# Optimization experiments

Hardware: AMD Instinct MI355X
Metric: run time of the kernel (lower is better)

Reference implementation:

```python
import jax, jax.numpy as jnp
import numpy as np

NUM_HEADS = 8
DIM_HEAD = 64
EMBED = NUM_HEADS * DIM_HEAD  # 512
B, S, L = 2, 128, 128


def setup_inputs() -> dict:
    key = jax.random.key(0)
    k1, k2 = jax.random.split(key)
    x = jax.random.normal(k1, (B, EMBED, S, L), dtype=jnp.float32)
    # 1x1 Conv2d == pointwise linear over channels: weight [3E, E], bias [3E]
    W = jax.random.normal(k2, (3 * EMBED, EMBED), dtype=jnp.float32) * (EMBED ** -0.5)
    b = jnp.zeros((3 * EMBED,), dtype=jnp.float32)
    return {"x": x, "W": W, "b": b}


def reference(x, W, b):
    Bsz, D, S_, L_ = x.shape
    H, Dh = NUM_HEADS, DIM_HEAD
    scale = Dh ** -0.5
    # QKV projection (1x1 conv)
    qkv = jnp.einsum('oi,bisl->bosl', W, x) + b[None, :, None, None]
    q, k, v = jnp.split(qkv, 3, axis=1)
    q = q.reshape(Bsz, H, Dh, S_, L_) * scale
    k = k.reshape(Bsz, H, Dh, S_, L_)
    v = v.reshape(Bsz, H, Dh, S_, L_)
    # Column attention: attend along S axis, independently per column l
    col_scores = jnp.einsum('bhdsl,bhdtl->bhlst', q, k)      # [B,H,L,S,S]
    col_attn = jax.nn.softmax(col_scores, axis=-1)
    out_col = jnp.einsum('bhlst,bhdtl->bhdsl', col_attn, v)  # [B,H,Dh,S,L]
    # Row attention: attend along L axis, independently per row s
    row_scores = jnp.einsum('bhdsl,bhdsm->bhslm', q, k)      # [B,H,S,L,L]
    row_attn = jax.nn.softmax(row_scores, axis=-1)
    out_row = jnp.einsum('bhslm,bhdsm->bhdsl', row_attn, v)  # [B,H,Dh,S,L]
    out = (out_col + out_row).reshape(Bsz, H * Dh, S_, L_)
    return out
```

## Files before the change

### kernel.cpp

```cpp
#include <hip/hip_runtime.h>
#include <stdint.h>

#define EMB 512
#define THREE_E 1536
#define SL 16384
#define K_DIM 512

typedef unsigned short ushort;
typedef short bf16x8 __attribute__((ext_vector_type(8)));
typedef float f32x4 __attribute__((ext_vector_type(4)));

__device__ __forceinline__ ushort f2bf(float f) {
  unsigned u = __float_as_uint(f);
  u += 0x7fffu + ((u >> 16) & 1u);
  return (ushort)(u >> 16);
}
__device__ __forceinline__ float bf2f(ushort s) {
  return __uint_as_float((unsigned)s << 16);
}

__device__ __forceinline__ void async16(const ushort* g, ushort* l) {
  __builtin_amdgcn_global_load_lds(
      (const __attribute__((address_space(1))) unsigned int*)g,
      (__attribute__((address_space(3))) unsigned int*)l, 16, 0, 0);
}

__global__ __launch_bounds__(256) void prep(const float* __restrict__ W,
                                            ushort* __restrict__ Wb,
                                            const float* __restrict__ x,
                                            ushort* __restrict__ xT) {
  __shared__ ushort t[64][68];
  const int bx = blockIdx.x;
  const int tid = threadIdx.x;
  if (bx < 768) {
    int i = bx * 256 + tid;
    float4 f = ((const float4*)W)[i];
    uint2 o;
    o.x = (unsigned)f2bf(f.x) | ((unsigned)f2bf(f.y) << 16);
    o.y = (unsigned)f2bf(f.z) | ((unsigned)f2bf(f.w) << 16);
    ((uint2*)Wb)[i] = o;
    return;
  }
  const int r = bx - 768;
  const int n0 = (r & 255) * 64;
  const int i0 = ((r >> 8) & 7) * 64;
  const int b = r >> 11;
  const float* xp = x + ((size_t)(b * EMB + i0)) * SL + n0;
  #pragma unroll
  for (int it = 0; it < 4; it++) {
    int f = it * 256 + tid;
    int rr = f >> 4, c4 = (f & 15) * 4;
    float4 v = *(const float4*)&xp[(size_t)rr * SL + c4];
    uint2 p;
    p.x = (unsigned)f2bf(v.x) | ((unsigned)f2bf(v.y) << 16);
    p.y = (unsigned)f2bf(v.z) | ((unsigned)f2bf(v.w) << 16);
    *(uint2*)&t[rr][c4] = p;
  }
  __syncthreads();
  ushort* op = xT + ((size_t)(b * SL + n0)) * EMB + i0;
  #pragma unroll
  for (int it = 0; it < 4; it++) {
    int u = it * 256 + tid;
    int n = u >> 4, i4 = (u & 15) * 4;
    uint2 p;
    ushort* ps = (ushort*)&p;
    #pragma unroll
    for (int j = 0; j < 4; j++) ps[j] = t[i4 + j][n];
    *(uint2*)&op[(size_t)n * EMB + i4] = p;
  }
}

__global__ __launch_bounds__(512, 2) void qkv_gemm(const ushort* __restrict__ Wb,
                                                   const ushort* __restrict__ xT,
                                                   const float* __restrict__ bias,
                                                   ushort* __restrict__ rowQ) {
  __shared__ __align__(16) char sm[131072];
  ushort* const A0 = (ushort*)sm;
  ushort* const B0 = (ushort*)(sm + 32768);
  ushort* const A1 = (ushort*)(sm + 65536);
  ushort* const B1 = (ushort*)(sm + 98304);
  const int tid = threadIdx.x;
  const int bz = blockIdx.z;
  const int m0 = blockIdx.y * 256;
  const int n0 = blockIdx.x * 256;
  const int lane = tid & 63, w = tid >> 6;
  const int wm = w >> 2, wn = w & 3;
  const int l15 = lane & 15, quad = lane >> 4;
  const int r8 = lane >> 3;
  const int cg8 = ((lane & 7) ^ r8) * 8;
  const int rx = l15 & 7;
  const ushort* Wt = Wb + (size_t)m0 * K_DIM;
  const ushort* Xt = xT + ((size_t)bz * SL + n0) * K_DIM;

  f32x4 acc[8][4] = {};
  bf16x8 av[4][2], bv0[2][2], bv1[2][2];

#define STG(gb, lb)                                                       \
  async16((gb) + (size_t)(w * 8 + r8) * K_DIM + cg8, (lb) + w * 512);     \
  async16((gb) + (size_t)(w * 8 + r8 + 64) * K_DIM + cg8, (lb) + w * 512 + 4096)

#define LDA(AP, MH)                                                           \
  _Pragma("unroll") for (int mt = 0; mt < 4; mt++) {                          \
    const int row = wm * 128 + (MH) * 64 + mt * 16 + l15;                     \
    av[mt][0] = *(const bf16x8*)&(AP)[row * 64 + ((quad ^ rx) * 8)];          \
    av[mt][1] = *(const bf16x8*)&(AP)[row * 64 + (((quad + 4) ^ rx) * 8)];    \
  }

#define LDB(BP, NH, BV)                                                       \
  _Pragma("unroll") for (int nt = 0; nt < 2; nt++) {                          \
    const int row = wn * 64 + (NH) * 32 + nt * 16 + l15;                      \
    BV[nt][0] = *(const bf16x8*)&(BP)[row * 64 + ((quad ^ rx) * 8)];          \
    BV[nt][1] = *(const bf16x8*)&(BP)[row * 64 + (((quad + 4) ^ rx) * 8)];    \
  }

#define MM(MH, NH, BV)                                                        \
  __builtin_amdgcn_s_setprio(1);                                              \
  _Pragma("unroll") for (int mt = 0; mt < 4; mt++)                            \
  _Pragma("unroll") for (int nt = 0; nt < 2; nt++) {                          \
    acc[(MH) * 4 + mt][(NH) * 2 + nt] =                                       \
        __builtin_amdgcn_mfma_f32_16x16x32_bf16(                              \
            av[mt][0], BV[nt][0], acc[(MH) * 4 + mt][(NH) * 2 + nt], 0, 0, 0);\
    acc[(MH) * 4 + mt][(NH) * 2 + nt] =                                       \
        __builtin_amdgcn_mfma_f32_16x16x32_bf16(                              \
            av[mt][1], BV[nt][1], acc[(MH) * 4 + mt][(NH) * 2 + nt], 0, 0, 0);\
  }                                                                           \
  __builtin_amdgcn_s_setprio(0)

#define BAR __builtin_amdgcn_s_barrier()
#define LGKM0 asm volatile("s_waitcnt lgkmcnt(0)" ::: "memory")
#define VMC(N) asm volatile("s_waitcnt vmcnt(" #N ")" ::: "memory")

  STG(Xt, B0);
  STG(Xt + 65536, B0 + 8192);
  STG(Wt, A0);
  STG(Wt + 65536, A0 + 8192);
  STG(Xt + 64, B1);
  STG(Xt + 65536 + 64, B1 + 8192);
  VMC(4);
  BAR;

  for (int t = 0; t < 4; ++t) {
    const int kB = t * 128 + 64;
    const int kN = t * 128 + 128;
    const int kN2 = t * 128 + 192;
    const bool st = (t < 3);
    LDA(A0, 0); LDB(B0, 0, bv0);
    STG(Wt + kB, A1);
    BAR; LGKM0; MM(0, 0, bv0); BAR;
    LDB(B0, 1, bv1);
    STG(Wt + 65536 + kB, A1 + 8192);
    BAR; LGKM0; MM(0, 1, bv1); BAR;
    LDA(A0, 1);
    if (st) { STG(Xt + kN, B0); }
    BAR; LGKM0; MM(1, 1, bv1); BAR;
    if (st) { STG(Xt + 65536 + kN, B0 + 8192); }
    BAR; MM(1, 0, bv0);
    if (t == 3) { VMC(0); } else { VMC(4); }
    BAR;
    LDA(A1, 0); LDB(B1, 0, bv0);
    if (st) { STG(Wt + kN, A0); }
    BAR; LGKM0; MM(0, 0, bv0); BAR;
    LDB(B1, 1, bv1);
    if (st) { STG(Wt + 65536 + kN, A0 + 8192); }
    BAR; LGKM0; MM(0, 1, bv1); BAR;
    LDA(A1, 1);
    if (st) { STG(Xt + kN2, B1); }
    BAR; LGKM0; MM(1, 1, bv1); BAR;
    if (st) { STG(Xt + 65536 + kN2, B1 + 8192); }
    BAR; MM(1, 0, bv0);
    if (st) { VMC(4); }
    BAR;
  }

  __syncthreads();
  {
    ushort* ep = (ushort*)sm + w * 4608;
    const float sc = (m0 < 512) ? 0.125f : 1.0f;
    const int q4 = quad * 4;
    const int sidx = (n0 >> 7) + (wn >> 1);
    const int lbase = (wn & 1) * 64;
    const int ml = (lane & 7) * 8;
    const int nlo = lane >> 3;
    #pragma unroll
    for (int mh = 0; mh < 2; ++mh) {
      if (mh) { LGKM0; }
      #pragma unroll
      for (int mt = 0; mt < 4; ++mt) {
        const int mloc = mt * 16 + q4;
        const int mg = m0 + wm * 128 + mh * 64 + mloc;
        const float b0 = bias[mg], b1 = bias[mg + 1];
        const float b2 = bias[mg + 2], b3 = bias[mg + 3];
        #pragma unroll
        for (int nt = 0; nt < 4; ++nt) {
          const f32x4 a = acc[mh * 4 + mt][nt];
          uint2 pk;
          pk.x = (unsigned)f2bf((a[0] + b0) * sc) | ((unsigned)f2bf((a[1] + b1) * sc) << 16);
          pk.y = (unsigned)f2bf((a[2] + b2) * sc) | ((unsigned)f2bf((a[3] + b3) * sc) << 16);
          *(uint2*)&ep[(nt * 16 + l15) * 72 + mloc] = pk;
        }
      }
      LGKM0;
      const int mb0 = m0 + wm * 128 + mh * 64;
      const int sel = mb0 >> 9;
      const int hh = (mb0 >> 6) & 7;
      ushort* db = rowQ + ((((size_t)(bz * 3 + sel) * 8 + hh) * 128 + sidx) * 128) * 64;
      #pragma unroll
      for (int it = 0; it < 8; ++it) {
        const int nl = it * 8 + nlo;
        *(uint4*)&db[(size_t)(lbase + nl) * 64 + ml] = *(const uint4*)&ep[nl * 72 + ml];
      }
    }
  }
#undef STG
#undef LDA
#undef LDB
#undef MM
#undef BAR
#undef LGKM0
#undef VMC
}

template <int COL>
__global__ __launch_bounds__(256) void attn3(const ushort* __restrict__ qkv,
                                             ushort* __restrict__ tmp,
                                             float* __restrict__ out) {
  __shared__ ushort Ks[128 * 64];
  __shared__ ushort Vt[64 * 136];
  __shared__ ushort Ps[64 * 136];
  const int tid = threadIdx.x;
  const int fixed = blockIdx.x;
  const int h = blockIdx.y, b = blockIdx.z;
  const int w = tid >> 6, lane = tid & 63, l15 = lane & 15, quad = lane >> 4;
  const size_t off = COL ? (size_t)fixed * 64 : (size_t)fixed * 8192;
  const size_t tstr = COL ? 8192 : 64;
  const ushort* Qg = qkv + ((size_t)(b * 3 + 0) * 8 + h) * 1048576 + off;
  const ushort* Kg = Qg + (size_t)8 * 1048576;
  const ushort* Vg = Qg + (size_t)16 * 1048576;
  ushort* tb = tmp + (size_t)(b * 8 + h) * 1048576;
  {
    int r8k = lane >> 3;
    int cgk = (lane & 7) ^ r8k;
    #pragma unroll
    for (int t = 0; t < 4; t++) {
      int seg = 4 * w + t;
      int row = seg * 8 + r8k;
      async16(&Kg[(size_t)row * tstr + cgk * 8], &Ks[seg * 512]);
    }
  }
  {
    int trow = tid >> 3, d0 = (tid & 7) * 8, dg = tid & 7;
    #pragma unroll
    for (int it = 0; it < 4; it++) {
      int t = trow + it * 32;
      uint4 vv = *(const uint4*)&Vg[(size_t)t * tstr + d0];
      ushort* vs = (ushort*)&vv;
      #pragma unroll
      for (int k = 0; k < 8; k++) {
        int i = (k + dg) & 7;
        Vt[(d0 + i) * 136 + t] = vs[i];
      }
    }
  }
  bf16x8 aq[2][2];
  #pragma unroll
  for (int c = 0; c < 2; c++) {
    const ushort* qp = Qg + (size_t)(c * 64 + w * 16 + l15) * tstr + quad * 8;
    aq[c][0] = *(const bf16x8*)qp;
    aq[c][1] = *(const bf16x8*)(qp + 32);
  }
  uint2 treg[2][4];
  if (!COL) {
    #pragma unroll
    for (int c = 0; c < 2; c++) {
      const ushort* tp = tb + (size_t)(c * 64 + w * 16 + l15) * 8192 + (size_t)fixed * 64 + quad * 4;
      #pragma unroll
      for (int mt = 0; mt < 4; mt++) treg[c][mt] = *(const uint2*)(tp + mt * 16);
    }
  }
  __syncthreads();
  const int rx = l15 & 7;
  #pragma unroll
  for (int c = 0; c < 2; c++) {
    f32x4 accS[8];
    #pragma unroll
    for (int nt = 0; nt < 8; nt++) {
      int row = nt * 16 + l15;
      bf16x8 bk0 = *(const bf16x8*)&Ks[row * 64 + ((quad ^ rx) * 8)];
      bf16x8 bk1 = *(const bf16x8*)&Ks[row * 64 + (((quad + 4) ^ rx) * 8)];
      f32x4 z = {0.f, 0.f, 0.f, 0.f};
      z = __builtin_amdgcn_mfma_f32_16x16x32_bf16(aq[c][0], bk0, z, 0, 0, 0);
      z = __builtin_amdgcn_mfma_f32_16x16x32_bf16(aq[c][1], bk1, z, 0, 0, 0);
      accS[nt] = z;
    }
    float inv[4];
    #pragma unroll
    for (int r = 0; r < 4; r++) {
      float mx = accS[0][r];
      #pragma unroll
      for (int nt = 1; nt < 8; nt++) mx = fmaxf(mx, accS[nt][r]);
      mx = fmaxf(mx, __shfl_xor(mx, 1));
      mx = fmaxf(mx, __shfl_xor(mx, 2));
      mx = fmaxf(mx, __shfl_xor(mx, 4));
      mx = fmaxf(mx, __shfl_xor(mx, 8));
      float s = 0.f;
      #pragma unroll
      for (int nt = 0; nt < 8; nt++) {
        float p = __builtin_amdgcn_exp2f((accS[nt][r] - mx) * 1.44269504088896f);
        accS[nt][r] = p;
        s += p;
      }
      s += __shfl_xor(s, 1);
      s += __shfl_xor(s, 2);
      s += __shfl_xor(s, 4);
      s += __shfl_xor(s, 8);
      inv[r] = 1.0f / s;
    }
    asm volatile("s_waitcnt lgkmcnt(0)" ::: "memory");
    #pragma unroll
    for (int nt = 0; nt < 8; nt++)
      #pragma unroll
      for (int r = 0; r < 4; r++)
        Ps[(w * 16 + quad * 4 + r) * 136 + nt * 16 + l15] = f2bf(accS[nt][r] * inv[r]);
    asm volatile("s_waitcnt lgkmcnt(0)" ::: "memory");
    f32x4 accO[4] = {{0.f,0.f,0.f,0.f},{0.f,0.f,0.f,0.f},{0.f,0.f,0.f,0.f},{0.f,0.f,0.f,0.f}};
    #pragma unroll
    for (int kf = 0; kf < 4; kf++) {
      bf16x8 p = *(const bf16x8*)&Ps[(w * 16 + l15) * 136 + kf * 32 + quad * 8];
      #pragma unroll
      for (int t4 = 0; t4 < 4; t4++) {
        bf16x8 v = *(const bf16x8*)&Vt[(t4 * 16 + l15) * 136 + kf * 32 + quad * 8];
        accO[t4] = COL ? __builtin_amdgcn_mfma_f32_16x16x32_bf16(p, v, accO[t4], 0, 0, 0)
                       : __builtin_amdgcn_mfma_f32_16x16x32_bf16(v, p, accO[t4], 0, 0, 0);
      }
    }
    if (COL) {
      ushort* tp = tb + (size_t)fixed * 8192 + c * 4096;
      #pragma unroll
      for (int t4 = 0; t4 < 4; t4++)
        #pragma unroll
        for (int r = 0; r < 4; r++)
          tp[(w * 16 + quad * 4 + r) * 64 + t4 * 16 + l15] = f2bf(accO[t4][r]);
    } else {
      float* ob = out + (size_t)(b * EMB + h * 64) * SL + (size_t)fixed * 128 + c * 64 + w * 16 + l15;
      #pragma unroll
      for (int t4 = 0; t4 < 4; t4++) {
        const ushort* tr = (const ushort*)&treg[c][t4];
        #pragma unroll
        for (int r = 0; r < 4; r++)
          ob[(size_t)(t4 * 16 + quad * 4 + r) * SL] = accO[t4][r] + bf2f(tr[r]);
      }
    }
  }
}

extern "C" void kernel_launch(void* const* d_in, const int* in_sizes, int n_in,
                              void* d_out, int out_size, void* d_ws, size_t ws_size,
                              hipStream_t stream) {
  const float* x = (const float*)d_in[0];
  const float* W = (const float*)d_in[1];
  const float* bias = (const float*)d_in[2];
  float* out = (float*)d_out;
  ushort* rowQ = (ushort*)d_ws;
  ushort* xT = (ushort*)((char*)d_ws + 100663296);
  ushort* tmp = (ushort*)((char*)d_ws + 100663296);
  ushort* Wb = (ushort*)((char*)d_ws + 134217728);

  hipLaunchKernelGGL(prep, dim3(4864), dim3(256), 0, stream, W, Wb, x, xT);
  hipLaunchKernelGGL(qkv_gemm, dim3(64, 6, 2), dim3(512), 0, stream, Wb, xT, bias, rowQ);
  hipLaunchKernelGGL(attn3<1>, dim3(128, 8, 2), dim3(256), 0, stream, rowQ, tmp, out);
  hipLaunchKernelGGL(attn3<0>, dim3(128, 8, 2), dim3(256), 0, stream, rowQ, tmp, out);
}
```

Measured before the change: 248.6 us.

## Alias P buffer onto K tile in LDS to raise attention occupancy

The attention kernel now computes both 64-row score chunks before any softmax work, then syncs and reuses the K tile's LDS as the P staging buffer with an XOR-swizzled 128-wide layout instead of a padded 136-wide array. This cuts shared memory per block so more blocks fit per CU, and launch bounds now request 4 blocks. The row-pass residual loads move inside each chunk's processing. Holding both score accumulators live raises register pressure, which the occupancy hint may turn into spills.

After: 260.4 us. +4.8%, slower.

```diff
diff --git a/kernel.cpp b/kernel.cpp
--- a/kernel.cpp
+++ b/kernel.cpp
@@ -221,12 +221,12 @@
 }
 
 template <int COL>
-__global__ __launch_bounds__(256) void attn3(const ushort* __restrict__ qkv,
-                                             ushort* __restrict__ tmp,
-                                             float* __restrict__ out) {
+__global__ __launch_bounds__(256, 4) void attn3(const ushort* __restrict__ qkv,
+                                                ushort* __restrict__ tmp,
+                                                float* __restrict__ out) {
   __shared__ ushort Ks[128 * 64];
   __shared__ ushort Vt[64 * 136];
-  __shared__ ushort Ps[64 * 136];
+  ushort* const Ps = Ks;
   const int tid = threadIdx.x;
   const int fixed = blockIdx.x;
   const int h = blockIdx.y, b = blockIdx.z;
@@ -268,89 +268,92 @@
     aq[c][0] = *(const bf16x8*)qp;
     aq[c][1] = *(const bf16x8*)(qp + 32);
   }
-  uint2 treg[2][4];
-  if (!COL) {
-    #pragma unroll
-    for (int c = 0; c < 2; c++) {
-      const ushort* tp = tb + (size_t)(c * 64 + w * 16 + l15) * 8192 + (size_t)fixed * 64 + quad * 4;
-      #pragma unroll
-      for (int mt = 0; mt < 4; mt++) treg[c][mt] = *(const uint2*)(tp + mt * 16);
-    }
-  }
   __syncthreads();
   const int rx = l15 & 7;
+  f32x4 accS0[8], accS1[8];
   #pragma unroll
-  for (int c = 0; c < 2; c++) {
-    f32x4 accS[8];
-    #pragma unroll
-    for (int nt = 0; nt < 8; nt++) {
-      int row = nt * 16 + l15;
-      bf16x8 bk0 = *(const bf16x8*)&Ks[row * 64 + ((quad ^ rx) * 8)];
-      bf16x8 bk1 = *(const bf16x8*)&Ks[row * 64 + (((quad + 4) ^ rx) * 8)];
-      f32x4 z = {0.f, 0.f, 0.f, 0.f};
-      z = __builtin_amdgcn_mfma_f32_16x16x32_bf16(aq[c][0], bk0, z, 0, 0, 0);
-      z = __builtin_amdgcn_mfma_f32_16x16x32_bf16(aq[c][1], bk1, z, 0, 0, 0);
-      accS[nt] = z;
-    }
-    float inv[4];
-    #pragma unroll
-    for (int r = 0; r < 4; r++) {
-      float mx = accS[0][r];
-      #pragma unroll
-      for (int nt = 1; nt < 8; nt++) mx = fmaxf(mx, accS[nt][r]);
-      mx = fmaxf(mx, __shfl_xor(mx, 1));
-      mx = fmaxf(mx, __shfl_xor(mx, 2));
-      mx = fmaxf(mx, __shfl_xor(mx, 4));
-      mx = fmaxf(mx, __shfl_xor(mx, 8));
-      float s = 0.f;
-      #pragma unroll
-      for (int nt = 0; nt < 8; nt++) {
-        float p = __builtin_amdgcn_exp2f((accS[nt][r] - mx) * 1.44269504088896f);
-        accS[nt][r] = p;
-        s += p;
-      }
-      s += __shfl_xor(s, 1);
-      s += __shfl_xor(s, 2);
-      s += __shfl_xor(s, 4);
-      s += __shfl_xor(s, 8);
-      inv[r] = 1.0f / s;
-    }
-    asm volatile("s_waitcnt lgkmcnt(0)" ::: "memory");
-    #pragma unroll
-    for (int nt = 0; nt < 8; nt++)
-      #pragma unroll
-      for (int r = 0; r < 4; r++)
-        Ps[(w * 16 + quad * 4 + r) * 136 + nt * 16 + l15] = f2bf(accS[nt][r] * inv[r]);
-    asm volatile("s_waitcnt lgkmcnt(0)" ::: "memory");
-    f32x4 accO[4] = {{0.f,0.f,0.f,0.f},{0.f,0.f,0.f,0.f},{0.f,0.f,0.f,0.f},{0.f,0.f,0.f,0.f}};
-    #pragma unroll
-    for (int kf = 0; kf < 4; kf++) {
-      bf16x8 p = *(const bf16x8*)&Ps[(w * 16 + l15) * 136 + kf * 32 + quad * 8];
-      #pragma unroll
-      for (int t4 = 0; t4 < 4; t4++) {
-        bf16x8 v = *(const bf16x8*)&Vt[(t4 * 16 + l15) * 136 + kf * 32 + quad * 8];
-        accO[t4] = COL ? __builtin_amdgcn_mfma_f32_16x16x32_bf16(p, v, accO[t4], 0, 0, 0)
-                       : __builtin_amdgcn_mfma_f32_16x16x32_bf16(v, p, accO[t4], 0, 0, 0);
-      }
-    }
-    if (COL) {
-      ushort* tp = tb + (size_t)fixed * 8192 + c * 4096;
-      #pragma unroll
-      for (int t4 = 0; t4 < 4; t4++)
-        #pragma unroll
-        for (int r = 0; r < 4; r++)
-          tp[(w * 16 + quad * 4 + r) * 64 + t4 * 16 + l15] = f2bf(accO[t4][r]);
-    } else {
-      float* ob = out + (size_t)(b * EMB + h * 64) * SL + (size_t)fixed * 128 + c * 64 + w * 16 + l15;
-      #pragma unroll
-      for (int t4 = 0; t4 < 4; t4++) {
-        const ushort* tr = (const ushort*)&treg[c][t4];
-        #pragma unroll
-        for (int r = 0; r < 4; r++)
-          ob[(size_t)(t4 * 16 + quad * 4 + r) * SL] = accO[t4][r] + bf2f(tr[r]);
-      }
-    }
-  }
+  for (int nt = 0; nt < 8; nt++) {
+    int row = nt * 16 + l15;
+    bf16x8 bk0 = *(const bf16x8*)&Ks[row * 64 + ((quad ^ rx) * 8)];
+    bf16x8 bk1 = *(const bf16x8*)&Ks[row * 64 + (((quad + 4) ^ rx) * 8)];
+    f32x4 z0 = {0.f, 0.f, 0.f, 0.f};
+    z0 = __builtin_amdgcn_mfma_f32_16x16x32_bf16(aq[0][0], bk0, z0, 0, 0, 0);
+    z0 = __builtin_amdgcn_mfma_f32_16x16x32_bf16(aq[0][1], bk1, z0, 0, 0, 0);
+    accS0[nt] = z0;
+    f32x4 z1 = {0.f, 0.f, 0.f, 0.f};
+    z1 = __builtin_amdgcn_mfma_f32_16x16x32_bf16(aq[1][0], bk0, z1, 0, 0, 0);
+    z1 = __builtin_amdgcn_mfma_f32_16x16x32_bf16(aq[1][1], bk1, z1, 0, 0, 0);
+    accS1[nt] = z1;
+  }
+  __syncthreads();
+
+#define PROCESS(ACCS, C)                                                      \
+  {                                                                           \
+    uint2 treg[4];                                                            \
+    if (!COL) {                                                               \
+      const ushort* tp = tb + (size_t)((C) * 64 + w * 16 + l15) * 8192 +      \
+                         (size_t)fixed * 64 + quad * 4;                       \
+      _Pragma("unroll") for (int mt = 0; mt < 4; mt++)                        \
+        treg[mt] = *(const uint2*)(tp + mt * 16);                             \
+    }                                                                         \
+    float inv[4];                                                             \
+    _Pragma("unroll") for (int r = 0; r < 4; r++) {                           \
+      float mx = ACCS[0][r];                                                  \
+      _Pragma("unroll") for (int nt = 1; nt < 8; nt++)                        \
+        mx = fmaxf(mx, ACCS[nt][r]);                                          \
+      mx = fmaxf(mx, __shfl_xor(mx, 1));                                      \
+      mx = fmaxf(mx, __shfl_xor(mx, 2));                                      \
+      mx = fmaxf(mx, __shfl_xor(mx, 4));                                      \
+      mx = fmaxf(mx, __shfl_xor(mx, 8));                                      \
+      float s = 0.f;                                                          \
+      _Pragma("unroll") for (int nt = 0; nt < 8; nt++) {                      \
+        float p = __builtin_amdgcn_exp2f((ACCS[nt][r] - mx) * 1.44269504088896f); \
+        ACCS[nt][r] = p;                                                      \
+        s += p;                                                               \
+      }                                                                       \
+      s += __shfl_xor(s, 1);                                                  \
+      s += __shfl_xor(s, 2);                                                  \
+      s += __shfl_xor(s, 4);                                                  \
+      s += __shfl_xor(s, 8);                                                  \
+      inv[r] = 1.0f / s;                                                      \
+    }                                                                         \
+    asm volatile("s_waitcnt lgkmcnt(0)" ::: "memory");                        \
+    _Pragma("unroll") for (int nt = 0; nt < 8; nt++)                          \
+      _Pragma("unroll") for (int r = 0; r < 4; r++)                           \
+        Ps[(w * 16 + quad * 4 + r) * 128 +                                    \
+           ((nt * 16 + l15) ^ (((quad * 4 + r) & 7) << 4))] =                 \
+            f2bf(ACCS[nt][r] * inv[r]);                                       \
+    asm volatile("s_waitcnt lgkmcnt(0)" ::: "memory");                        \
+    f32x4 accO[4] = {{0.f, 0.f, 0.f, 0.f}, {0.f, 0.f, 0.f, 0.f},              \
+                     {0.f, 0.f, 0.f, 0.f}, {0.f, 0.f, 0.f, 0.f}};             \
+    _Pragma("unroll") for (int kf = 0; kf < 4; kf++) {                        \
+      bf16x8 p = *(const bf16x8*)&Ps[(w * 16 + l15) * 128 +                   \
+                                     ((kf * 32 + quad * 8) ^ ((l15 & 7) << 4))]; \
+      _Pragma("unroll") for (int t4 = 0; t4 < 4; t4++) {                      \
+        bf16x8 v = *(const bf16x8*)&Vt[(t4 * 16 + l15) * 136 + kf * 32 + quad * 8]; \
+        accO[t4] = COL ? __builtin_amdgcn_mfma_f32_16x16x32_bf16(p, v, accO[t4], 0, 0, 0) \
+                       : __builtin_amdgcn_mfma_f32_16x16x32_bf16(v, p, accO[t4], 0, 0, 0); \
+      }                                                                       \
+    }                                                                         \
+    if (COL) {                                                                \
+      ushort* tp2 = tb + (size_t)fixed * 8192 + (C) * 4096;                   \
+      _Pragma("unroll") for (int t4 = 0; t4 < 4; t4++)                        \
+        _Pragma("unroll") for (int r = 0; r < 4; r++)                         \
+          tp2[(w * 16 + quad * 4 + r) * 64 + t4 * 16 + l15] = f2bf(accO[t4][r]); \
+    } else {                                                                  \
+      float* ob = out + (size_t)(b * EMB + h * 64) * SL + (size_t)fixed * 128 + \
+                  (C) * 64 + w * 16 + l15;                                    \
+      _Pragma("unroll") for (int t4 = 0; t4 < 4; t4++) {                      \
+        const ushort* tr = (const ushort*)&treg[t4];                          \
+        _Pragma("unroll") for (int r = 0; r < 4; r++)                         \
+          ob[(size_t)(t4 * 16 + quad * 4 + r) * SL] = accO[t4][r] + bf2f(tr[r]); \
+      }                                                                       \
+    }                                                                         \
+  }
+
+  PROCESS(accS0, 0);
+  PROCESS(accS1, 1);
+#undef PROCESS
 }
 
 extern "C" void kernel_launch(void* const* d_in, const int* in_sizes, int n_in,
```
